# Performance work log

Measured on AMD Instinct MI355X. Metric: run time of the kernel, lower is better.

The kernel has to match this reference:

```python
import jax, jax.numpy as jnp
import numpy as np

DIM = 192
HEADS = 6
HEAD_DIM = DIM // HEADS
K = 3          # kernel_size
PAD = 1
STRIDE = 2
SCALE = HEAD_DIM ** -0.5
B, H, W = 16, 56, 56


def setup_inputs() -> dict:
    key = jax.random.key(0)
    ks = jax.random.split(key, 6)
    x = jax.random.normal(ks[0], (B, H, W, DIM), jnp.float32)
    # Linear weights stored as [in, out] so y = x @ W + b (== torch x @ W.T)
    Wv = jax.random.normal(ks[1], (DIM, DIM), jnp.float32) * 0.05          # v_pj, no bias
    Wa = jax.random.normal(ks[2], (DIM, K**4 * HEADS), jnp.float32) * 0.05  # attn linear
    ba = jax.random.normal(ks[3], (K**4 * HEADS,), jnp.float32) * 0.01
    Wp = jax.random.normal(ks[4], (DIM, DIM), jnp.float32) * 0.05           # proj
    bp = jax.random.normal(ks[5], (DIM,), jnp.float32) * 0.01
    return {"x": x, "Wv": Wv, "Wa": Wa, "ba": ba, "Wp": Wp, "bp": bp}


def reference(x, Wv, Wa, ba, Wp, bp):
    # Dropout layers act as identity (eval mode).
    Bn, Hn, Wn, C = x.shape
    h = -(-Hn // STRIDE)  # ceil(H/stride) = 28
    w = -(-Wn // STRIDE)
    KK = K * K

    # --- value projection + unfold (im2col over K x K window, stride STRIDE) ---
    v = x @ Wv  # [B,H,W,C]
    vp = jnp.pad(v, ((0, 0), (PAD, PAD), (PAD, PAD), (0, 0)))
    # patches: [B,h,w,K*K,C]; loop is over the fixed 3x3 kernel taps only
    patches = jnp.stack(
        [vp[:, i:i + STRIDE * h:STRIDE, j:j + STRIDE * w:STRIDE, :]
         for i in range(K) for j in range(K)], axis=3)
    patches = patches.reshape(Bn, h * w, KK, HEADS, HEAD_DIM)

    # --- attention weights from avg-pooled map (H divisible by STRIDE here) ---
    pooled = x.reshape(Bn, h, STRIDE, w, STRIDE, C).mean(axis=(2, 4))  # [B,h,w,C]
    a = pooled.reshape(Bn, h * w, C) @ Wa + ba                         # [B,hw,K^4*heads]
    a = a.reshape(Bn, h * w, HEADS, KK, KK) * SCALE
    a = jax.nn.softmax(a, axis=-1)

    # --- windowed attention: [B,hw,heads,K2,K2] x [B,hw,K2,heads,hd] ---
    out = jnp.einsum('bnhpq,bnqhd->bnphd', a, patches)  # [B,hw,K2,heads,hd]
    out = out.reshape(Bn, h, w, KK, C)

    # --- fold (scatter-add of overlapping patches back to HxW) ---
    acc = jnp.zeros((Bn, Hn + 2 * PAD, Wn + 2 * PAD, C), x.dtype)
    idx = 0
    for i in range(K):
        for j in range(K):
            acc = acc.at[:, i:i + STRIDE * h:STRIDE, j:j + STRIDE * w:STRIDE, :].add(out[:, :, :, idx, :])
            idx += 1
    y = acc[:, PAD:PAD + Hn, PAD:PAD + Wn, :]

    return y @ Wp + bp
```

## Files before the change

kernel.cpp:

```cpp
#include <hip/hip_runtime.h>
#include <cstdint>
#include <cstddef>

#define DIMC    192
#define NHEADS  6
#define NATT    486
#define NB      16
#define NH      56
#define NWW     56
#define HPOOL   28
#define WPOOL   28
#define NPIX    784
#define VH      58
#define VW      58
#define MROWS   (NB*NH*NWW)
#define MPOOL   (NB*NPIX)
#define SCALE_A 0.17677669529663687f

using bf16x8 = __attribute__((ext_vector_type(8))) short;
using f32x4  = __attribute__((ext_vector_type(4))) float;

static __device__ __forceinline__ unsigned short f2bf(float f) {
    unsigned int u = __float_as_uint(f);
    unsigned int r = (u + 0x7fffu + ((u >> 16) & 1u)) >> 16;
    return (unsigned short)r;
}
static __device__ __forceinline__ float bf2f(unsigned short u) {
    return __uint_as_float((unsigned int)u << 16);
}

__global__ __launch_bounds__(256)
void wt_convert_kernel(const float* __restrict__ Wv, const float* __restrict__ Wp,
                       const float* __restrict__ Wa,
                       unsigned short* __restrict__ WTv, unsigned short* __restrict__ WTp,
                       unsigned short* __restrict__ WaT)
{
    int idx = blockIdx.x * 256 + threadIdx.x;
    if (idx < 73728) {
        int sel = idx / 36864;
        int r   = idx - sel * 36864;
        int n   = r / DIMC;
        int k   = r - n * DIMC;
        const float* W = sel ? Wp : Wv;
        unsigned short* WT = sel ? WTp : WTv;
        WT[r] = f2bf(W[k * DIMC + n]);
    } else {
        int r = idx - 73728;
        int n = r / DIMC;
        int k = r - n * DIMC;
        WaT[r] = (n < NATT) ? f2bf(Wa[(size_t)k * NATT + n] * SCALE_A) : (unsigned short)0;
    }
}

__global__ __launch_bounds__(256)
void vp_border_zero_kernel(unsigned int* __restrict__ vpu)
{
    int idx = blockIdx.x * 256 + threadIdx.x;
    if (idx >= 350208) return;
    int cu   = idx % 96;
    int rest = idx / 96;
    int b    = rest / 228;
    int p    = rest - b * 228;
    int hi, wi;
    if (p < 58)       { hi = 0;  wi = p; }
    else if (p < 116) { hi = 57; wi = p - 58; }
    else { int q = p - 116; hi = 1 + (q >> 1); wi = (q & 1) * 57; }
    vpu[(((size_t)b * VH + hi) * VW + wi) * 96 + cu] = 0u;
}

template<int MODE>
__global__ __launch_bounds__(256)
void mfma_gemm_kernel(const void* __restrict__ Av, const unsigned short* __restrict__ WT,
                      const float* __restrict__ bias, void* __restrict__ Cv)
{
    __shared__ unsigned short As[64 * DIMC];

    const int t  = threadIdx.x;
    const int l  = t & 63;
    const int w  = t >> 6;
    const int wr = w >> 1;
    const int wc = w & 1;
    const int by = blockIdx.x;

    if (MODE == 0) {
        const float* Ab = (const float*)Av + (size_t)by * 64 * DIMC;
#pragma unroll
        for (int i = 0; i < 12; ++i) {
            int f = i * 1024 + t * 4;
            float4 v = *(const float4*)(Ab + f);
            int row = f / DIMC;
            int k   = f - row * DIMC;
            ushort4 u;
            u.x = f2bf(v.x); u.y = f2bf(v.y); u.z = f2bf(v.z); u.w = f2bf(v.w);
            int off = (row * 384 + k * 2) ^ ((row & 7) << 4);
            *(ushort4*)((char*)As + off) = u;
        }
    } else {
        const unsigned short* Ab = (const unsigned short*)Av + (size_t)by * 64 * DIMC;
#pragma unroll
        for (int i = 0; i < 6; ++i) {
            int f = i * 2048 + t * 8;
            bf16x8 v = *(const bf16x8*)(Ab + f);
            int row = f / DIMC;
            int k   = f - row * DIMC;
            int off = (row * 384 + k * 2) ^ ((row & 7) << 4);
            *(bf16x8*)((char*)As + off) = v;
        }
    }
    __syncthreads();

    f32x4 acc[2][6];
#pragma unroll
    for (int mi = 0; mi < 2; ++mi)
#pragma unroll
        for (int ni = 0; ni < 6; ++ni) acc[mi][ni] = (f32x4)0.f;

    const int arow0 = wr * 32 + (l & 15);
    const int kb    = (l >> 4) << 4;

#pragma unroll
    for (int ks = 0; ks < 6; ++ks) {
        bf16x8 a[2], b[6];
#pragma unroll
        for (int mi = 0; mi < 2; ++mi) {
            int row = arow0 + mi * 16;
            int off = (row * 384 + ks * 64 + kb) ^ ((row & 7) << 4);
            a[mi] = *(const bf16x8*)((const char*)As + off);
        }
#pragma unroll
        for (int ni = 0; ni < 6; ++ni) {
            int n = wc * 96 + ni * 16 + (l & 15);
            b[ni] = *(const bf16x8*)(WT + (size_t)n * DIMC + ks * 32 + ((l >> 4) << 3));
        }
#pragma unroll
        for (int mi = 0; mi < 2; ++mi)
#pragma unroll
            for (int ni = 0; ni < 6; ++ni)
                acc[mi][ni] = __builtin_amdgcn_mfma_f32_16x16x32_bf16(
                    a[mi], b[ni], acc[mi][ni], 0, 0, 0);
    }

#pragma unroll
    for (int mi = 0; mi < 2; ++mi) {
#pragma unroll
        for (int r = 0; r < 4; ++r) {
            int m = by * 64 + wr * 32 + mi * 16 + ((l >> 4) << 2) + r;
            if (MODE == 1) {
                float* dst = (float*)Cv + (size_t)m * DIMC;
#pragma unroll
                for (int ni = 0; ni < 6; ++ni) {
                    int col = wc * 96 + ni * 16 + (l & 15);
                    dst[col] = acc[mi][ni][r] + bias[col];
                }
            } else {
                int bb = m / (NH * NWW);
                int rr = m - bb * (NH * NWW);
                int hi = rr / NWW;
                int wi = rr - hi * NWW;
                unsigned short* dst = (unsigned short*)Cv +
                    (((size_t)bb * VH + hi + 1) * VW + (wi + 1)) * DIMC;
#pragma unroll
                for (int ni = 0; ni < 6; ++ni) {
                    int col = wc * 96 + ni * 16 + (l & 15);
                    dst[col] = f2bf(acc[mi][ni][r]);
                }
            }
        }
    }
}

__global__ __launch_bounds__(512)
void pool_attn_mfma_kernel(const float* __restrict__ x, const unsigned short* __restrict__ WaT,
                           const float* __restrict__ ba, float* __restrict__ attn)
{
    __shared__ unsigned short As[64 * DIMC];
    __shared__ float Cs[16][489];
    __shared__ float ba_s[NATT];

    const int t  = threadIdx.x;
    const int l  = t & 63;
    const int w  = t >> 6;
    const int wr = w >> 2;
    const int wc = w & 3;
    const int by = blockIdx.x;

    if (t < NATT) ba_s[t] = ba[t] * SCALE_A;

#pragma unroll
    for (int i = 0; i < 6; ++i) {
        int f   = i * 2048 + t * 4;
        int row = f / DIMC;
        int k   = f - row * DIMC;
        int m   = by * 64 + row;
        int b   = m / NPIX;
        int r   = m - b * NPIX;
        int hh  = r / WPOOL;
        int ww  = r - hh * WPOOL;
        const float* xp = x + (((size_t)(b * NH + hh * 2)) * NWW + ww * 2) * DIMC + k;
        float4 v0 = *(const float4*)(xp);
        float4 v1 = *(const float4*)(xp + DIMC);
        float4 v2 = *(const float4*)(xp + (size_t)NWW * DIMC);
        float4 v3 = *(const float4*)(xp + (size_t)NWW * DIMC + DIMC);
        ushort4 u;
        u.x = f2bf(0.25f * (v0.x + v1.x + v2.x + v3.x));
        u.y = f2bf(0.25f * (v0.y + v1.y + v2.y + v3.y));
        u.z = f2bf(0.25f * (v0.z + v1.z + v2.z + v3.z));
        u.w = f2bf(0.25f * (v0.w + v1.w + v2.w + v3.w));
        int off = (row * 384 + k * 2) ^ ((row & 7) << 4);
        *(ushort4*)((char*)As + off) = u;
    }
    __syncthreads();

    f32x4 acc[2][8];
#pragma unroll
    for (int mi = 0; mi < 2; ++mi)
#pragma unroll
        for (int ni = 0; ni < 8; ++ni) acc[mi][ni] = (f32x4)0.f;

    const int arow0 = wr * 32 + (l & 15);
    const int kb    = (l >> 4) << 4;

#pragma unroll
    for (int ks = 0; ks < 6; ++ks) {
        bf16x8 a[2], b[8];
#pragma unroll
        for (int mi = 0; mi < 2; ++mi) {
            int row = arow0 + mi * 16;
            int off = (row * 384 + ks * 64 + kb) ^ ((row & 7) << 4);
            a[mi] = *(const bf16x8*)((const char*)As + off);
        }
#pragma unroll
        for (int ni = 0; ni < 8; ++ni) {
            int n = wc * 128 + ni * 16 + (l & 15);
            b[ni] = *(const bf16x8*)(WaT + (size_t)n * DIMC + ks * 32 + ((l >> 4) << 3));
        }
#pragma unroll
        for (int mi = 0; mi < 2; ++mi)
#pragma unroll
            for (int ni = 0; ni < 8; ++ni)
                acc[mi][ni] = __builtin_amdgcn_mfma_f32_16x16x32_bf16(
                    a[mi], b[ni], acc[mi][ni], 0, 0, 0);
    }

#pragma unroll
    for (int r0 = 0; r0 < 64; r0 += 16) {
        const int mi = (r0 >> 4) & 1;
        if (wr == (r0 >> 5)) {
#pragma unroll
            for (int ni = 0; ni < 8; ++ni) {
                int col = wc * 128 + ni * 16 + (l & 15);
                if (col < NATT) {
#pragma unroll
                    for (int r = 0; r < 4; ++r)
                        Cs[((l >> 4) << 2) + r][col] =
                            (mi == 0 ? acc[0][ni][r] : acc[1][ni][r]) + ba_s[col];
                }
            }
        }
        __syncthreads();
        for (int g = t; g < 864; g += 512) {
            int lr = g / 54;
            int gc = (g - lr * 54) * 9;
            const float* ap = &Cs[lr][gc];
            float mx = ap[0];
#pragma unroll
            for (int q = 1; q < 9; ++q) mx = fmaxf(mx, ap[q]);
            float e[9];
            float sum = 0.f;
#pragma unroll
            for (int q = 0; q < 9; ++q) { e[q] = __expf(ap[q] - mx); sum += e[q]; }
            float inv = 1.f / sum;
            int m = by * 64 + r0 + lr;
            float* dst = attn + (size_t)m * NATT + gc;
#pragma unroll
            for (int q = 0; q < 9; ++q) dst[q] = e[q] * inv;
        }
        __syncthreads();
    }
}

template<int NI, int NJ>
static __device__ __forceinline__ void gather_body(
    int b, int p, int qc, int head, int c,
    const float* __restrict__ attn, const unsigned short* __restrict__ vp,
    unsigned short* __restrict__ y)
{
    const int pr = p >> 1;
    const int qr = qc >> 1;

    float accx = 0.f, accy = 0.f;

#pragma unroll
    for (int wi = 0; wi < NI; ++wi) {
        const int  hh  = (NI == 1) ? pr : (wi == 0 ? pr : pr + 1);
        const bool hv  = (NI == 1) || (wi == 0) || (pr + 1 < HPOOL);
        const int  hhs = hv ? hh : (HPOOL - 1);
        const int  iof = (NI == 1) ? 1 : (wi == 0 ? 2 : 0);
#pragma unroll
        for (int wj = 0; wj < NJ; ++wj) {
            const int  ww  = (NJ == 1) ? qr : (wj == 0 ? qr : qr + 1);
            const bool wv  = (NJ == 1) || (wj == 0) || (qr + 1 < WPOOL);
            const int  wws = wv ? ww : (WPOOL - 1);
            const bool ok  = hv && wv;
            const int  jof = (NJ == 1) ? 1 : (wj == 0 ? 2 : 0);

            const float* ap = attn +
                ((size_t)(b * NPIX + hhs * WPOOL + wws) * NATT + head * 81 + (iof * 3 + jof) * 9);
            float a[9];
#pragma unroll
            for (int k = 0; k < 9; ++k) a[k] = ok ? ap[k] : 0.f;

            const unsigned short* vb = vp +
                (((size_t)(b * VH + 2 * hhs)) * VW + 2 * wws) * DIMC + c;
            ushort2 v[9];
#pragma unroll
            for (int qi = 0; qi < 3; ++qi)
#pragma unroll
                for (int qj = 0; qj < 3; ++qj)
                    v[qi * 3 + qj] = *(const ushort2*)(vb + ((size_t)qi * VW + qj) * DIMC);

#pragma unroll
            for (int k = 0; k < 9; ++k) {
                accx = fmaf(a[k], bf2f(v[k].x), accx);
                accy = fmaf(a[k], bf2f(v[k].y), accy);
            }
        }
    }
    size_t pix = (size_t)b * (NH * NWW) + (size_t)p * NWW + qc;
    ushort2 r;
    r.x = f2bf(accx);
    r.y = f2bf(accy);
    *(ushort2*)(y + pix * DIMC + c) = r;
}

__global__ __launch_bounds__(192)
void gather_kernel(const float* __restrict__ attn, const unsigned short* __restrict__ vp,
                   unsigned short* __restrict__ y)
{
    const int t    = threadIdx.x;
    const int pl   = t / 96;
    const int c2   = t - pl * 96;
    const int c    = c2 * 2;
    const int head = c2 >> 4;

    const int flat = blockIdx.x;
    const int wgid = (flat & 7) * 3136 + (flat >> 3);
    const int b    = wgid / 1568;
    const int rr   = wgid - b * 1568;
    const int p    = rr / 28;
    const int wq   = rr - p * 28;
    const int qc   = wq + pl * 28;

    if (p & 1) {
        if (wq & 1) gather_body<2, 2>(b, p, qc, head, c, attn, vp, y);
        else        gather_body<2, 1>(b, p, qc, head, c, attn, vp, y);
    } else {
        if (wq & 1) gather_body<1, 2>(b, p, qc, head, c, attn, vp, y);
        else        gather_body<1, 1>(b, p, qc, head, c, attn, vp, y);
    }
}

extern "C" void kernel_launch(void* const* d_in, const int* in_sizes, int n_in,
                              void* d_out, int out_size, void* d_ws, size_t ws_size,
                              hipStream_t stream)
{
    const float* x  = (const float*)d_in[0];
    const float* Wv = (const float*)d_in[1];
    const float* Wa = (const float*)d_in[2];
    const float* ba = (const float*)d_in[3];
    const float* Wp = (const float*)d_in[4];
    const float* bp = (const float*)d_in[5];
    float* out = (float*)d_out;

    const size_t vp_elems   = (size_t)NB * VH * VW * DIMC;
    const size_t attn_elems = (size_t)MPOOL * NATT;
    const size_t y_elems    = (size_t)MROWS * DIMC;

    unsigned short* vp   = (unsigned short*)d_ws;
    float*          attn = (float*)(vp + vp_elems);
    unsigned short* y    = (unsigned short*)(attn + attn_elems);
    unsigned short* WTv  = y + y_elems;
    unsigned short* WTp  = WTv + 36864;
    unsigned short* WaT  = WTp + 36864;

    vp_border_zero_kernel<<<1369, 256, 0, stream>>>((unsigned int*)vp);
    wt_convert_kernel<<<672, 256, 0, stream>>>(Wv, Wp, Wa, WTv, WTp, WaT);

    mfma_gemm_kernel<0><<<MROWS / 64, 256, 0, stream>>>(x, WTv, nullptr, vp);
    pool_attn_mfma_kernel<<<MPOOL / 64, 512, 0, stream>>>(x, WaT, ba, attn);

    gather_kernel<<<25088, 192, 0, stream>>>(attn, vp, y);

    mfma_gemm_kernel<1><<<MROWS / 64, 256, 0, stream>>>(y, WTp, bp, out);
}
```

Measured before the change: 123.2 us.

## Stage GEMM epilogues through LDS for vector stores; store attention weights in bf16

Both GEMM epilogues now write their accumulators into shared memory first and then emit 16-byte vectorized global stores (bf16x8 for the padded value map, float4 with bias for the output), replacing scattered 2- and 4-byte stores. The softmax attention weights are stored as bf16 instead of fp32, which halves the attn buffer traffic written by the pool kernel and read by the gather kernel. The costs are extra barriers and shared-memory round trips in the epilogues, and lower precision for the attention weights.

```diff
diff --git a/kernel.cpp b/kernel.cpp
--- a/kernel.cpp
+++ b/kernel.cpp
@@ -140,38 +140,74 @@
                     a[mi], b[ni], acc[mi][ni], 0, 0, 0);
     }
 
-#pragma unroll
-    for (int mi = 0; mi < 2; ++mi) {
-#pragma unroll
-        for (int r = 0; r < 4; ++r) {
-            int m = by * 64 + wr * 32 + mi * 16 + ((l >> 4) << 2) + r;
-            if (MODE == 1) {
-                float* dst = (float*)Cv + (size_t)m * DIMC;
+    if (MODE == 0) {
+        __syncthreads();
+#pragma unroll
+        for (int mi = 0; mi < 2; ++mi) {
+#pragma unroll
+            for (int r = 0; r < 4; ++r) {
+                int row = wr * 32 + mi * 16 + ((l >> 4) << 2) + r;
 #pragma unroll
                 for (int ni = 0; ni < 6; ++ni) {
                     int col = wc * 96 + ni * 16 + (l & 15);
-                    dst[col] = acc[mi][ni][r] + bias[col];
-                }
-            } else {
-                int bb = m / (NH * NWW);
-                int rr = m - bb * (NH * NWW);
-                int hi = rr / NWW;
-                int wi = rr - hi * NWW;
-                unsigned short* dst = (unsigned short*)Cv +
-                    (((size_t)bb * VH + hi + 1) * VW + (wi + 1)) * DIMC;
-#pragma unroll
-                for (int ni = 0; ni < 6; ++ni) {
-                    int col = wc * 96 + ni * 16 + (l & 15);
-                    dst[col] = f2bf(acc[mi][ni][r]);
+                    As[row * DIMC + col] = f2bf(acc[mi][ni][r]);
                 }
             }
         }
+        __syncthreads();
+#pragma unroll
+        for (int i = 0; i < 6; ++i) {
+            int f   = i * 2048 + t * 8;
+            int row = f / DIMC;
+            int k   = f - row * DIMC;
+            int m   = by * 64 + row;
+            int bb  = m / (NH * NWW);
+            int rr  = m - bb * (NH * NWW);
+            int hi  = rr / NWW;
+            int wi  = rr - hi * NWW;
+            bf16x8 v = *(const bf16x8*)&As[f];
+            unsigned short* dst = (unsigned short*)Cv +
+                (((size_t)bb * VH + hi + 1) * VW + (wi + 1)) * DIMC + k;
+            *(bf16x8*)dst = v;
+        }
+    } else {
+        float* fAs = (float*)As;
+#pragma unroll
+        for (int chunk = 0; chunk < 2; ++chunk) {
+            __syncthreads();
+            if (wr == chunk) {
+#pragma unroll
+                for (int mi = 0; mi < 2; ++mi) {
+#pragma unroll
+                    for (int r = 0; r < 4; ++r) {
+                        int rowl = mi * 16 + ((l >> 4) << 2) + r;
+#pragma unroll
+                        for (int ni = 0; ni < 6; ++ni) {
+                            int col = wc * 96 + ni * 16 + (l & 15);
+                            fAs[rowl * DIMC + col] = acc[mi][ni][r];
+                        }
+                    }
+                }
+            }
+            __syncthreads();
+#pragma unroll
+            for (int i = 0; i < 6; ++i) {
+                int f   = i * 1024 + t * 4;
+                int row = f / DIMC;
+                int k   = f - row * DIMC;
+                int m   = by * 64 + chunk * 32 + row;
+                float4 v  = *(const float4*)&fAs[f];
+                float4 bv = *(const float4*)&bias[k];
+                v.x += bv.x; v.y += bv.y; v.z += bv.z; v.w += bv.w;
+                *(float4*)((float*)Cv + (size_t)m * DIMC + k) = v;
+            }
+        }
     }
 }
 
 __global__ __launch_bounds__(512)
 void pool_attn_mfma_kernel(const float* __restrict__ x, const unsigned short* __restrict__ WaT,
-                           const float* __restrict__ ba, float* __restrict__ attn)
+                           const float* __restrict__ ba, unsigned short* __restrict__ attn)
 {
     __shared__ unsigned short As[64 * DIMC];
     __shared__ float Cs[16][489];
@@ -271,9 +307,9 @@
             for (int q = 0; q < 9; ++q) { e[q] = __expf(ap[q] - mx); sum += e[q]; }
             float inv = 1.f / sum;
             int m = by * 64 + r0 + lr;
-            float* dst = attn + (size_t)m * NATT + gc;
-#pragma unroll
-            for (int q = 0; q < 9; ++q) dst[q] = e[q] * inv;
+            unsigned short* dst = attn + (size_t)m * NATT + gc;
+#pragma unroll
+            for (int q = 0; q < 9; ++q) dst[q] = f2bf(e[q] * inv);
         }
         __syncthreads();
     }
@@ -282,7 +318,7 @@
 template<int NI, int NJ>
 static __device__ __forceinline__ void gather_body(
     int b, int p, int qc, int head, int c,
-    const float* __restrict__ attn, const unsigned short* __restrict__ vp,
+    const unsigned short* __restrict__ attn, const unsigned short* __restrict__ vp,
     unsigned short* __restrict__ y)
 {
     const int pr = p >> 1;
@@ -292,23 +328,23 @@
 
 #pragma unroll
     for (int wi = 0; wi < NI; ++wi) {
-        const int  hh  = (NI == 1) ? pr : (wi == 0 ? pr : pr + 1);
+        const int  hh  = pr + wi;
         const bool hv  = (NI == 1) || (wi == 0) || (pr + 1 < HPOOL);
         const int  hhs = hv ? hh : (HPOOL - 1);
         const int  iof = (NI == 1) ? 1 : (wi == 0 ? 2 : 0);
 #pragma unroll
         for (int wj = 0; wj < NJ; ++wj) {
-            const int  ww  = (NJ == 1) ? qr : (wj == 0 ? qr : qr + 1);
+            const int  ww  = qr + wj;
             const bool wv  = (NJ == 1) || (wj == 0) || (qr + 1 < WPOOL);
             const int  wws = wv ? ww : (WPOOL - 1);
             const bool ok  = hv && wv;
             const int  jof = (NJ == 1) ? 1 : (wj == 0 ? 2 : 0);
 
-            const float* ap = attn +
+            const unsigned short* ap = attn +
                 ((size_t)(b * NPIX + hhs * WPOOL + wws) * NATT + head * 81 + (iof * 3 + jof) * 9);
             float a[9];
 #pragma unroll
-            for (int k = 0; k < 9; ++k) a[k] = ok ? ap[k] : 0.f;
+            for (int k = 0; k < 9; ++k) a[k] = ok ? bf2f(ap[k]) : 0.f;
 
             const unsigned short* vb = vp +
                 (((size_t)(b * VH + 2 * hhs)) * VW + 2 * wws) * DIMC + c;
@@ -334,7 +370,8 @@
 }
 
 __global__ __launch_bounds__(192)
-void gather_kernel(const float* __restrict__ attn, const unsigned short* __restrict__ vp,
+void gather_kernel(const unsigned short* __restrict__ attn,
+                   const unsigned short* __restrict__ vp,
                    unsigned short* __restrict__ y)
 {
     const int t    = threadIdx.x;
@@ -377,8 +414,8 @@
     const size_t y_elems    = (size_t)MROWS * DIMC;
 
     unsigned short* vp   = (unsigned short*)d_ws;
-    float*          attn = (float*)(vp + vp_elems);
-    unsigned short* y    = (unsigned short*)(attn + attn_elems);
+    unsigned short* attn = vp + vp_elems;
+    unsigned short* y    = attn + attn_elems;
     unsigned short* WTv  = y + y_elems;
     unsigned short* WTp  = WTv + 36864;
     unsigned short* WaT  = WTp + 36864;
```

New measurement: 139.4 us. 13.2% more time.
